# Optimization experiments

Measured on AMD Instinct MI355X. Metric: run time of the kernel, lower is better.

## Reference

```python
import jax, jax.numpy as jnp
import numpy as np

HIDDEN = 1024
NUM_HEADS = 16
HEAD_DIM = HIDDEN // NUM_HEADS
WINDOW = 512


def setup_inputs() -> dict:
    key = jax.random.key(0)
    ks = jax.random.split(key, 6)
    b, s = 2, 4096
    x = jax.random.normal(ks[0], (b, s, HIDDEN), dtype=jnp.float32)
    attention_mask = jnp.ones((b, s), dtype=jnp.int32)
    scale = 1.0 / np.sqrt(HIDDEN)
    Wq = jax.random.normal(ks[1], (HIDDEN, HIDDEN), dtype=jnp.float32) * scale
    Wk = jax.random.normal(ks[2], (HIDDEN, HIDDEN), dtype=jnp.float32) * scale
    Wv = jax.random.normal(ks[3], (HIDDEN, HIDDEN), dtype=jnp.float32) * scale
    Wo = jax.random.normal(ks[4], (HIDDEN, HIDDEN), dtype=jnp.float32) * scale
    return {"x": x, "attention_mask": attention_mask,
            "Wq": Wq, "Wk": Wk, "Wv": Wv, "Wo": Wo}


def reference(x, attention_mask, Wq, Wk, Wv, Wo):
    b, s, d = x.shape
    # nn.Linear computes x @ W.T
    q = (x @ Wq.T).reshape(b, s, NUM_HEADS, HEAD_DIM).transpose(0, 2, 1, 3)
    k = (x @ Wk.T).reshape(b, s, NUM_HEADS, HEAD_DIM).transpose(0, 2, 1, 3)
    v = (x @ Wv.T).reshape(b, s, NUM_HEADS, HEAD_DIM).transpose(0, 2, 1, 3)
    # [b,h,s,s] scores
    scores = jnp.einsum('bhqd,bhkd->bhqk', q, k) / np.sqrt(HEAD_DIM)
    # causal sliding-window mask: allow j <= i and j >= i - window + 1
    i = jnp.arange(s)[:, None]
    j = jnp.arange(s)[None, :]
    window_mask = (j <= i) & (j >= i - WINDOW + 1)  # [s,s]
    neg_inf = jnp.finfo(scores.dtype).min
    scores = jnp.where(window_mask[None, None], scores, neg_inf)
    pad = attention_mask.astype(bool)[:, None, None, :]  # [b,1,1,s]
    scores = jnp.where(pad, scores, neg_inf)
    probs = jax.nn.softmax(scores, axis=-1)
    out = jnp.einsum('bhqk,bhkd->bhqd', probs, v)
    out = out.transpose(0, 2, 1, 3).reshape(b, s, d)
    return out @ Wo.T
```

## Files before the change

kernel.cpp:

```cpp
#include <hip/hip_runtime.h>
#include <cstdint>
#include <cstddef>

#define HID 1024
#define SEQ 4096
#define NB  2
#define NH  16
#define HD  64
#define WIN 512
#define TOK (NB*SEQ)

typedef _Float16 f16x8 __attribute__((ext_vector_type(8)));
typedef _Float16 f16x4 __attribute__((ext_vector_type(4)));
typedef float    f32x4 __attribute__((ext_vector_type(4)));

__global__ __launch_bounds__(256)
void convert_kernel(const float* __restrict__ X, const float* __restrict__ w0,
                    const float* __restrict__ w1, const float* __restrict__ w2,
                    const float* __restrict__ w3,
                    _Float16* __restrict__ Xh, _Float16* __restrict__ Wh) {
  const int bi = blockIdx.x;
  const float* src; _Float16* dst; size_t off;
  if (bi < 4096) {
    src = X; dst = Xh; off = (size_t)bi * 2048;
  } else {
    const int wi = bi - 4096, z = wi >> 9;
    src = (z == 0) ? w0 : (z == 1) ? w1 : (z == 2) ? w2 : w3;
    dst = Wh + (size_t)z * HID * HID;
    off = (size_t)(wi & 511) * 2048;
  }
  const size_t i = off + (size_t)threadIdx.x * 8;
  f32x4 a = *(const f32x4*)(src + i);
  f32x4 b = *(const f32x4*)(src + i + 4);
  f16x8 o;
#pragma unroll
  for (int r = 0; r < 4; ++r) { o[r] = (_Float16)a[r]; o[r+4] = (_Float16)b[r]; }
  *(f16x8*)(dst + i) = o;
}

__device__ __forceinline__ void gload16(const void* g, void* lds) {
  __builtin_amdgcn_global_load_lds(
      (__attribute__((address_space(1))) void*)(void*)g,
      (__attribute__((address_space(3))) void*)lds, 16, 0, 0);
}

__device__ __forceinline__ void gemm_mainloop(
    const _Float16* __restrict__ A, const _Float16* __restrict__ W,
    _Float16* sA, _Float16* sB, f32x4 (&acc)[4][4], int m0, int n0) {
  const int tid  = threadIdx.x;
  const int lane = tid & 63;
  const int wave = tid >> 6;
  const int wm = wave >> 1, wn = wave & 1;
  const int l15 = lane & 15, quad = lane >> 4;

  const int o0 = tid * 16;
  const int o1 = o0 + 4096;
  const _Float16* a0 = A + (size_t)(m0 + (o0 >> 6)) * HID + ((o0 & 63) >> 1);
  const _Float16* a1 = A + (size_t)(m0 + (o1 >> 6)) * HID + ((o1 & 63) >> 1);
  const _Float16* w0 = W + (size_t)(n0 + (o0 >> 6)) * HID + ((o0 & 63) >> 1);
  const _Float16* w1 = W + (size_t)(n0 + (o1 >> 6)) * HID + ((o1 & 63) >> 1);
  _Float16* la0 = sA + (o0 >> 1);
  _Float16* la1 = sA + (o1 >> 1);
  _Float16* lb0 = sB + (o0 >> 1);
  _Float16* lb1 = sB + (o1 >> 1);

  const int aoff = (wm*64 + l15)*32 + quad*8;
  const int boff = (wn*64 + l15)*32 + quad*8;

  for (int k0 = 0; k0 < HID; k0 += 64) {
    __syncthreads();
    gload16(a0 + k0,      la0);
    gload16(a1 + k0,      la1);
    gload16(a0 + k0 + 32, la0 + 4096);
    gload16(a1 + k0 + 32, la1 + 4096);
    gload16(w0 + k0,      lb0);
    gload16(w1 + k0,      lb1);
    gload16(w0 + k0 + 32, lb0 + 4096);
    gload16(w1 + k0 + 32, lb1 + 4096);
    __syncthreads();
#pragma unroll
    for (int s = 0; s < 2; ++s) {
      const int sb = s * 4096;
      f16x8 af[4], wf[4];
#pragma unroll
      for (int t = 0; t < 4; ++t) {
        af[t] = *(const f16x8*)(sA + sb + aoff + t*512);
        wf[t] = *(const f16x8*)(sB + sb + boff + t*512);
      }
#pragma unroll
      for (int i = 0; i < 4; ++i)
#pragma unroll
        for (int j = 0; j < 4; ++j)
          acc[i][j] = __builtin_amdgcn_mfma_f32_16x16x32_f16(af[i], wf[j], acc[i][j], 0, 0, 0);
    }
  }
}

__global__ __launch_bounds__(256, 3)
void gemm_qkv_kernel(const _Float16* __restrict__ X,
                     const _Float16* __restrict__ Wh,
                     _Float16* __restrict__ Q,
                     _Float16* __restrict__ Kb,
                     _Float16* __restrict__ Vt) {
  __shared__ __align__(16) _Float16 sA[128*64];
  __shared__ __align__(16) _Float16 sB[128*64];
  const int i  = blockIdx.x;
  const int g  = i & 7;
  const int j  = i >> 3;
  const int mi = j & 7;
  const int c  = j >> 3;
  const int z  = c >> 3;
  const int n0 = (c & 7) * 128;
  const int m0 = (g*8 + mi) * 128;
  const _Float16* W = Wh + (size_t)z * HID * HID;
  f32x4 acc[4][4] = {};
  gemm_mainloop(X, W, sA, sB, acc, m0, n0);

  const int tid  = threadIdx.x;
  const int lane = tid & 63;
  const int wave = tid >> 6;
  const int wm = wave >> 1, wn = wave & 1;
  const int l15 = lane & 15, quad = lane >> 4;

  if (z < 2) {
    _Float16* C = (z == 0) ? Q : Kb;
    const float scl = (z == 0) ? 0.18033688011f : 1.0f;
#pragma unroll
    for (int tm = 0; tm < 4; ++tm)
#pragma unroll
      for (int tn = 0; tn < 4; ++tn) {
        const int row = m0 + wm*64 + tm*16 + quad*4;
        const int col = n0 + wn*64 + tn*16 + l15;
#pragma unroll
        for (int r = 0; r < 4; ++r)
          C[(size_t)(row + r)*HID + col] = (_Float16)(acc[tm][tn][r] * scl);
      }
  } else {
#pragma unroll
    for (int tm = 0; tm < 4; ++tm)
#pragma unroll
      for (int tn = 0; tn < 4; ++tn) {
        const int row = m0 + wm*64 + tm*16 + quad*4;
        const int col = n0 + wn*64 + tn*16 + l15;
        f16x4 v;
#pragma unroll
        for (int r = 0; r < 4; ++r) v[r] = (_Float16)acc[tm][tn][r];
        *(f16x4*)(Vt + (size_t)col*TOK + row) = v;
      }
  }
}

__global__ __launch_bounds__(256, 3)
void gemm_o_kernel(const _Float16* __restrict__ A,
                   const _Float16* __restrict__ Wo,
                   float* __restrict__ C) {
  __shared__ __align__(16) _Float16 sA[128*64];
  __shared__ __align__(16) _Float16 sB[128*64];
  const int i  = blockIdx.x;
  const int g  = i & 7;
  const int j  = i >> 3;
  const int mi = j & 7;
  const int n0 = (j >> 3) * 128;
  const int m0 = (g*8 + mi) * 128;
  f32x4 acc[4][4] = {};
  gemm_mainloop(A, Wo, sA, sB, acc, m0, n0);

  const int tid  = threadIdx.x;
  const int lane = tid & 63;
  const int wave = tid >> 6;
  const int wm = wave >> 1, wn = wave & 1;
  const int l15 = lane & 15, quad = lane >> 4;
#pragma unroll
  for (int tm = 0; tm < 4; ++tm)
#pragma unroll
    for (int tn = 0; tn < 4; ++tn) {
      const int row = m0 + wm*64 + tm*16 + quad*4;
      const int col = n0 + wn*64 + tn*16 + l15;
#pragma unroll
      for (int r = 0; r < 4; ++r)
        C[(size_t)(row + r)*HID + col] = acc[tm][tn][r];
    }
}

__global__ __launch_bounds__(512, 4)
void attn_kernel(const _Float16* __restrict__ Q, const _Float16* __restrict__ Kb,
                 const _Float16* __restrict__ Vt, const int* __restrict__ AM,
                 _Float16* __restrict__ O) {
  __shared__ __align__(16) _Float16 sK[128*64];
  __shared__ __align__(16) _Float16 sV[64*128];
  __shared__ __align__(16) _Float16 sP[8*32*64];
  __shared__ int sOK;

  const int bi = blockIdx.x;
  const int g  = bi & 7;
  const int jj = bi >> 3;
  const int combo = g*4 + (jj >> 4);
  const int h = combo & 15, b = combo >> 4;
  const int qb = jj & 15;

  const int tid  = threadIdx.x;
  const int lane = tid & 63, wave = tid >> 6;
  const int l15 = lane & 15, quad = lane >> 4;

  const int q0 = qb * 256;
  const int qw = q0 + wave * 32;

  const int swz = l15 & 7;
  const int cA8 = ((quad ^ swz) << 3);
  const int cB8 = (((quad + 4) ^ swz) << 3);

  f16x8 qf[2][2];
#pragma unroll
  for (int ns = 0; ns < 2; ++ns) {
    const size_t qbse = (size_t)(b*SEQ + qw + ns*16 + l15)*HID + h*HD + quad*8;
    qf[ns][0] = *(const f16x8*)(Q + qbse);
    qf[ns][1] = *(const f16x8*)(Q + qbse + 32);
  }

  int stage_lo = (q0 - (WIN - 1));
  stage_lo = (stage_lo < 0) ? 0 : (stage_lo & ~127);
  const int nst = (q0 + 256 - stage_lo) >> 7;

  if (tid == 0) sOK = 1;
  __syncthreads();
  {
    int ok = 1;
    for (int j = stage_lo + tid; j < q0 + 256; j += 512) ok &= (AM[b*SEQ + j] != 0);
    if (!ok) sOK = 0;
  }
  __syncthreads();
  const bool allok = (sOK != 0);

  const int prow = tid >> 3;
  const int pc   = tid & 7;
  const int pco  = ((pc ^ (prow & 7)) << 3);
  f16x8 pk0, pk1, pv0, pv1;
  {
    const _Float16* kp = Kb + (size_t)(b*SEQ + stage_lo + prow)*HID + h*HD + pco;
    pk0 = *(const f16x8*)kp;
    pk1 = *(const f16x8*)(kp + (size_t)64*HID);
    const _Float16* vp = Vt + (size_t)(h*HD + prow)*TOK + b*SEQ + stage_lo + pco;
    pv0 = *(const f16x8*)vp;
    pv1 = *(const f16x8*)(vp + 64);
  }

  float l_run[2] = {0.0f, 0.0f};
  f32x4 o[4][2] = {};
  _Float16* myP = sP + wave * (32*64);

  for (int st = 0; st < nst; ++st) {
    const int j0st = stage_lo + st*128;
    __syncthreads();
    *(f16x8*)(sK + prow*64 + pc*8)        = pk0;
    *(f16x8*)(sK + (64 + prow)*64 + pc*8) = pk1;
    *(f16x8*)(sV + prow*128 + pc*8)       = pv0;
    *(f16x8*)(sV + prow*128 + 64 + pc*8)  = pv1;
    __syncthreads();
    if (st + 1 < nst) {
      const int jn = j0st + 128;
      const _Float16* kp = Kb + (size_t)(b*SEQ + jn + prow)*HID + h*HD + pco;
      pk0 = *(const f16x8*)kp;
      pk1 = *(const f16x8*)(kp + (size_t)64*HID);
      const _Float16* vp = Vt + (size_t)(h*HD + prow)*TOK + b*SEQ + jn + pco;
      pv0 = *(const f16x8*)vp;
      pv1 = *(const f16x8*)(vp + 64);
    }

#pragma unroll
    for (int s = 0; s < 2; ++s) {
      const int j0 = j0st + s*64;
      if (j0 > qw + 31 || j0 + 63 < qw - (WIN - 1)) continue;
      const bool interior = (j0 + 63 <= qw) && (j0 >= qw - (WIN - 32));

      f32x4 sc[4][2] = {};
#pragma unroll
      for (int t = 0; t < 4; ++t) {
        const f16x8 kf0 = *(const f16x8*)(sK + (s*64 + t*16 + l15)*64 + cA8);
        const f16x8 kf1 = *(const f16x8*)(sK + (s*64 + t*16 + l15)*64 + cB8);
        sc[t][0] = __builtin_amdgcn_mfma_f32_16x16x32_f16(kf0, qf[0][0], sc[t][0], 0, 0, 0);
        sc[t][0] = __builtin_amdgcn_mfma_f32_16x16x32_f16(kf1, qf[0][1], sc[t][0], 0, 0, 0);
        sc[t][1] = __builtin_amdgcn_mfma_f32_16x16x32_f16(kf0, qf[1][0], sc[t][1], 0, 0, 0);
        sc[t][1] = __builtin_amdgcn_mfma_f32_16x16x32_f16(kf1, qf[1][1], sc[t][1], 0, 0, 0);
      }

      if (!allok) {
#pragma unroll
        for (int t = 0; t < 4; ++t)
#pragma unroll
          for (int r = 0; r < 4; ++r) {
            const float ad = (AM[b*SEQ + j0 + t*16 + quad*4 + r] == 0) ? -2e30f : 0.0f;
            sc[t][0][r] += ad;
            sc[t][1][r] += ad;
          }
      }

#pragma unroll
      for (int ns = 0; ns < 2; ++ns) {
        if (!interior) {
          const int i = qw + ns*16 + l15;
#pragma unroll
          for (int t = 0; t < 4; ++t)
#pragma unroll
            for (int r = 0; r < 4; ++r) {
              const int j = j0 + t*16 + quad*4 + r;
              const bool valid = (unsigned)(i - j) < WIN;
              sc[t][ns][r] = valid ? sc[t][ns][r] : -1e30f;
            }
        }
        float sum = 0.0f;
#pragma unroll
        for (int t = 0; t < 4; ++t) {
          f16x4 pvv;
#pragma unroll
          for (int r = 0; r < 4; ++r) {
            const float p = __builtin_amdgcn_exp2f(sc[t][ns][r]);
            sum += p;
            pvv[r] = (_Float16)p;
          }
          const int paddr = (ns*16 + l15)*64 + (((2*t + (quad >> 1)) ^ swz) << 3) + (quad & 1)*4;
          *(f16x4*)(myP + paddr) = pvv;
        }
        sum += __shfl_xor(sum, 16, 64);
        sum += __shfl_xor(sum, 32, 64);
        l_run[ns] += sum;
      }

      const f16x8 pf00 = *(const f16x8*)(myP + l15*64 + cA8);
      const f16x8 pf01 = *(const f16x8*)(myP + l15*64 + cB8);
      const f16x8 pf10 = *(const f16x8*)(myP + (16 + l15)*64 + cA8);
      const f16x8 pf11 = *(const f16x8*)(myP + (16 + l15)*64 + cB8);
#pragma unroll
      for (int dt = 0; dt < 4; ++dt) {
        const f16x8 vf0 = *(const f16x8*)(sV + (dt*16 + l15)*128 + s*64 + cA8);
        const f16x8 vf1 = *(const f16x8*)(sV + (dt*16 + l15)*128 + s*64 + cB8);
        o[dt][0] = __builtin_amdgcn_mfma_f32_16x16x32_f16(vf0, pf00, o[dt][0], 0, 0, 0);
        o[dt][0] = __builtin_amdgcn_mfma_f32_16x16x32_f16(vf1, pf01, o[dt][0], 0, 0, 0);
        o[dt][1] = __builtin_amdgcn_mfma_f32_16x16x32_f16(vf0, pf10, o[dt][1], 0, 0, 0);
        o[dt][1] = __builtin_amdgcn_mfma_f32_16x16x32_f16(vf1, pf11, o[dt][1], 0, 0, 0);
      }
    }
  }

  const float inv[2] = {1.0f / fmaxf(l_run[0], 1e-30f), 1.0f / fmaxf(l_run[1], 1e-30f)};
#pragma unroll
  for (int ns = 0; ns < 2; ++ns) {
    const size_t ob = (size_t)(b*SEQ + qw + ns*16 + l15)*HID + h*HD + quad*4;
#pragma unroll
    for (int dt = 0; dt < 4; ++dt) {
      f16x4 v;
#pragma unroll
      for (int r = 0; r < 4; ++r) v[r] = (_Float16)(o[dt][ns][r] * inv[ns]);
      *(f16x4*)(O + ob + dt*16) = v;
    }
  }
}

extern "C" void kernel_launch(void* const* d_in, const int* in_sizes, int n_in,
                              void* d_out, int out_size, void* d_ws, size_t ws_size,
                              hipStream_t stream) {
  const float* X  = (const float*)d_in[0];
  const int*   AM = (const int*)d_in[1];
  const float* Wq = (const float*)d_in[2];
  const float* Wk = (const float*)d_in[3];
  const float* Wv = (const float*)d_in[4];
  const float* Wo = (const float*)d_in[5];
  float* out = (float*)d_out;

  _Float16* Xh = (_Float16*)d_ws;
  _Float16* Wh = Xh + (size_t)TOK*HID;
  _Float16* Qb = Wh + (size_t)4*HID*HID;
  _Float16* Kb = Qb + (size_t)TOK*HID;
  _Float16* Vt = Kb + (size_t)TOK*HID;
  _Float16* AO = Vt + (size_t)TOK*HID;

  convert_kernel<<<dim3(4096 + 4*512), dim3(256), 0, stream>>>(X, Wq, Wk, Wv, Wo, Xh, Wh);
  gemm_qkv_kernel<<<dim3(1536), dim3(256), 0, stream>>>(Xh, Wh, Qb, Kb, Vt);
  attn_kernel<<<dim3(512), dim3(512), 0, stream>>>(Qb, Kb, Vt, AM, AO);
  gemm_o_kernel<<<dim3(512), dim3(256), 0, stream>>>(AO, Wh + (size_t)3*HID*HID, out);
}
```

Measured before the change: 217.6 us.

## Load K/V fragments directly from global per wave, drop shared staging

The attention kernel no longer stages K and V tiles through shared memory with block-wide barriers. Each wave now loads its K and V MFMA fragments straight from global memory (relying on L2 for reuse) and walks only the 64-key tiles in its own window. Blocks shrink to 256 threads covering 128 queries, with 1024 blocks, and the padding-mask check becomes a per-wave vote. This removes the barriers and LDS traffic, but each wave loads K/V redundantly, there is no prefetch across iterations, and the K rows are read with strided global accesses.

Result: slower. 274.6 us (+26.2%).

```diff
diff --git a/kernel.cpp b/kernel.cpp
--- a/kernel.cpp
+++ b/kernel.cpp
@@ -182,28 +182,24 @@
     }
 }
 
-__global__ __launch_bounds__(512, 4)
+__global__ __launch_bounds__(256, 3)
 void attn_kernel(const _Float16* __restrict__ Q, const _Float16* __restrict__ Kb,
                  const _Float16* __restrict__ Vt, const int* __restrict__ AM,
                  _Float16* __restrict__ O) {
-  __shared__ __align__(16) _Float16 sK[128*64];
-  __shared__ __align__(16) _Float16 sV[64*128];
-  __shared__ __align__(16) _Float16 sP[8*32*64];
-  __shared__ int sOK;
+  __shared__ __align__(16) _Float16 sP[4*32*64];
 
   const int bi = blockIdx.x;
   const int g  = bi & 7;
   const int jj = bi >> 3;
-  const int combo = g*4 + (jj >> 4);
+  const int combo = g*4 + (jj >> 5);
   const int h = combo & 15, b = combo >> 4;
-  const int qb = jj & 15;
+  const int qt = jj & 31;
 
   const int tid  = threadIdx.x;
   const int lane = tid & 63, wave = tid >> 6;
   const int l15 = lane & 15, quad = lane >> 4;
 
-  const int q0 = qb * 256;
-  const int qw = q0 + wave * 32;
+  const int qw = qt*128 + wave*32;
 
   const int swz = l15 & 7;
   const int cA8 = ((quad ^ swz) << 3);
@@ -217,127 +213,99 @@
     qf[ns][1] = *(const f16x8*)(Q + qbse + 32);
   }
 
-  int stage_lo = (q0 - (WIN - 1));
-  stage_lo = (stage_lo < 0) ? 0 : (stage_lo & ~127);
-  const int nst = (q0 + 256 - stage_lo) >> 7;
-
-  if (tid == 0) sOK = 1;
-  __syncthreads();
-  {
-    int ok = 1;
-    for (int j = stage_lo + tid; j < q0 + 256; j += 512) ok &= (AM[b*SEQ + j] != 0);
-    if (!ok) sOK = 0;
-  }
-  __syncthreads();
-  const bool allok = (sOK != 0);
-
-  const int prow = tid >> 3;
-  const int pc   = tid & 7;
-  const int pco  = ((pc ^ (prow & 7)) << 3);
-  f16x8 pk0, pk1, pv0, pv1;
-  {
-    const _Float16* kp = Kb + (size_t)(b*SEQ + stage_lo + prow)*HID + h*HD + pco;
-    pk0 = *(const f16x8*)kp;
-    pk1 = *(const f16x8*)(kp + (size_t)64*HID);
-    const _Float16* vp = Vt + (size_t)(h*HD + prow)*TOK + b*SEQ + stage_lo + pco;
-    pv0 = *(const f16x8*)vp;
-    pv1 = *(const f16x8*)(vp + 64);
-  }
+  int lo = qw - (WIN - 1); if (lo < 0) lo = 0;
+  const int kt_lo = lo >> 6;
+  const int kt_hi = (qw + 31) >> 6;
+
+  int okl = 1;
+  for (int j = kt_lo*64 + lane; j < (kt_hi + 1)*64; j += 64)
+    okl &= (AM[b*SEQ + j] != 0);
+  const bool allok = __all(okl);
 
   float l_run[2] = {0.0f, 0.0f};
   f32x4 o[4][2] = {};
   _Float16* myP = sP + wave * (32*64);
 
-  for (int st = 0; st < nst; ++st) {
-    const int j0st = stage_lo + st*128;
-    __syncthreads();
-    *(f16x8*)(sK + prow*64 + pc*8)        = pk0;
-    *(f16x8*)(sK + (64 + prow)*64 + pc*8) = pk1;
-    *(f16x8*)(sV + prow*128 + pc*8)       = pv0;
-    *(f16x8*)(sV + prow*128 + 64 + pc*8)  = pv1;
-    __syncthreads();
-    if (st + 1 < nst) {
-      const int jn = j0st + 128;
-      const _Float16* kp = Kb + (size_t)(b*SEQ + jn + prow)*HID + h*HD + pco;
-      pk0 = *(const f16x8*)kp;
-      pk1 = *(const f16x8*)(kp + (size_t)64*HID);
-      const _Float16* vp = Vt + (size_t)(h*HD + prow)*TOK + b*SEQ + jn + pco;
-      pv0 = *(const f16x8*)vp;
-      pv1 = *(const f16x8*)(vp + 64);
-    }
-
-#pragma unroll
-    for (int s = 0; s < 2; ++s) {
-      const int j0 = j0st + s*64;
-      if (j0 > qw + 31 || j0 + 63 < qw - (WIN - 1)) continue;
-      const bool interior = (j0 + 63 <= qw) && (j0 >= qw - (WIN - 32));
-
-      f32x4 sc[4][2] = {};
+  for (int kt = kt_lo; kt <= kt_hi; ++kt) {
+    const int j0 = kt * 64;
+    const bool interior = (j0 + 63 <= qw) && (j0 >= qw - (WIN - 32));
+
+    f16x8 kf[4][2];
+#pragma unroll
+    for (int t = 0; t < 4; ++t) {
+      const _Float16* kp = Kb + (size_t)(b*SEQ + j0 + t*16 + l15)*HID + h*HD + quad*8;
+      kf[t][0] = *(const f16x8*)kp;
+      kf[t][1] = *(const f16x8*)(kp + 32);
+    }
+    f16x8 vf[4][2];
+#pragma unroll
+    for (int dt = 0; dt < 4; ++dt) {
+      const _Float16* vp = Vt + (size_t)(h*HD + dt*16 + l15)*TOK + b*SEQ + j0 + quad*8;
+      vf[dt][0] = *(const f16x8*)vp;
+      vf[dt][1] = *(const f16x8*)(vp + 32);
+    }
+
+    f32x4 sc[4][2] = {};
+#pragma unroll
+    for (int t = 0; t < 4; ++t) {
+      sc[t][0] = __builtin_amdgcn_mfma_f32_16x16x32_f16(kf[t][0], qf[0][0], sc[t][0], 0, 0, 0);
+      sc[t][0] = __builtin_amdgcn_mfma_f32_16x16x32_f16(kf[t][1], qf[0][1], sc[t][0], 0, 0, 0);
+      sc[t][1] = __builtin_amdgcn_mfma_f32_16x16x32_f16(kf[t][0], qf[1][0], sc[t][1], 0, 0, 0);
+      sc[t][1] = __builtin_amdgcn_mfma_f32_16x16x32_f16(kf[t][1], qf[1][1], sc[t][1], 0, 0, 0);
+    }
+
+    if (!allok) {
+#pragma unroll
+      for (int t = 0; t < 4; ++t)
+#pragma unroll
+        for (int r = 0; r < 4; ++r) {
+          const float ad = (AM[b*SEQ + j0 + t*16 + quad*4 + r] == 0) ? -2e30f : 0.0f;
+          sc[t][0][r] += ad;
+          sc[t][1][r] += ad;
+        }
+    }
+
+#pragma unroll
+    for (int ns = 0; ns < 2; ++ns) {
+      if (!interior) {
+        const int i = qw + ns*16 + l15;
+#pragma unroll
+        for (int t = 0; t < 4; ++t)
+#pragma unroll
+          for (int r = 0; r < 4; ++r) {
+            const int j = j0 + t*16 + quad*4 + r;
+            const bool valid = (unsigned)(i - j) < WIN;
+            sc[t][ns][r] = valid ? sc[t][ns][r] : -1e30f;
+          }
+      }
+      float sum = 0.0f;
 #pragma unroll
       for (int t = 0; t < 4; ++t) {
-        const f16x8 kf0 = *(const f16x8*)(sK + (s*64 + t*16 + l15)*64 + cA8);
-        const f16x8 kf1 = *(const f16x8*)(sK + (s*64 + t*16 + l15)*64 + cB8);
-        sc[t][0] = __builtin_amdgcn_mfma_f32_16x16x32_f16(kf0, qf[0][0], sc[t][0], 0, 0, 0);
-        sc[t][0] = __builtin_amdgcn_mfma_f32_16x16x32_f16(kf1, qf[0][1], sc[t][0], 0, 0, 0);
-        sc[t][1] = __builtin_amdgcn_mfma_f32_16x16x32_f16(kf0, qf[1][0], sc[t][1], 0, 0, 0);
-        sc[t][1] = __builtin_amdgcn_mfma_f32_16x16x32_f16(kf1, qf[1][1], sc[t][1], 0, 0, 0);
-      }
-
-      if (!allok) {
-#pragma unroll
-        for (int t = 0; t < 4; ++t)
-#pragma unroll
-          for (int r = 0; r < 4; ++r) {
-            const float ad = (AM[b*SEQ + j0 + t*16 + quad*4 + r] == 0) ? -2e30f : 0.0f;
-            sc[t][0][r] += ad;
-            sc[t][1][r] += ad;
-          }
-      }
-
-#pragma unroll
-      for (int ns = 0; ns < 2; ++ns) {
-        if (!interior) {
-          const int i = qw + ns*16 + l15;
-#pragma unroll
-          for (int t = 0; t < 4; ++t)
-#pragma unroll
-            for (int r = 0; r < 4; ++r) {
-              const int j = j0 + t*16 + quad*4 + r;
-              const bool valid = (unsigned)(i - j) < WIN;
-              sc[t][ns][r] = valid ? sc[t][ns][r] : -1e30f;
-            }
+        f16x4 pvv;
+#pragma unroll
+        for (int r = 0; r < 4; ++r) {
+          const float p = __builtin_amdgcn_exp2f(sc[t][ns][r]);
+          sum += p;
+          pvv[r] = (_Float16)p;
         }
-        float sum = 0.0f;
-#pragma unroll
-        for (int t = 0; t < 4; ++t) {
-          f16x4 pvv;
-#pragma unroll
-          for (int r = 0; r < 4; ++r) {
-            const float p = __builtin_amdgcn_exp2f(sc[t][ns][r]);
-            sum += p;
-            pvv[r] = (_Float16)p;
-          }
-          const int paddr = (ns*16 + l15)*64 + (((2*t + (quad >> 1)) ^ swz) << 3) + (quad & 1)*4;
-          *(f16x4*)(myP + paddr) = pvv;
-        }
-        sum += __shfl_xor(sum, 16, 64);
-        sum += __shfl_xor(sum, 32, 64);
-        l_run[ns] += sum;
-      }
-
-      const f16x8 pf00 = *(const f16x8*)(myP + l15*64 + cA8);
-      const f16x8 pf01 = *(const f16x8*)(myP + l15*64 + cB8);
-      const f16x8 pf10 = *(const f16x8*)(myP + (16 + l15)*64 + cA8);
-      const f16x8 pf11 = *(const f16x8*)(myP + (16 + l15)*64 + cB8);
-#pragma unroll
-      for (int dt = 0; dt < 4; ++dt) {
-        const f16x8 vf0 = *(const f16x8*)(sV + (dt*16 + l15)*128 + s*64 + cA8);
-        const f16x8 vf1 = *(const f16x8*)(sV + (dt*16 + l15)*128 + s*64 + cB8);
-        o[dt][0] = __builtin_amdgcn_mfma_f32_16x16x32_f16(vf0, pf00, o[dt][0], 0, 0, 0);
-        o[dt][0] = __builtin_amdgcn_mfma_f32_16x16x32_f16(vf1, pf01, o[dt][0], 0, 0, 0);
-        o[dt][1] = __builtin_amdgcn_mfma_f32_16x16x32_f16(vf0, pf10, o[dt][1], 0, 0, 0);
-        o[dt][1] = __builtin_amdgcn_mfma_f32_16x16x32_f16(vf1, pf11, o[dt][1], 0, 0, 0);
-      }
+        const int paddr = (ns*16 + l15)*64 + (((2*t + (quad >> 1)) ^ swz) << 3) + (quad & 1)*4;
+        *(f16x4*)(myP + paddr) = pvv;
+      }
+      sum += __shfl_xor(sum, 16, 64);
+      sum += __shfl_xor(sum, 32, 64);
+      l_run[ns] += sum;
+    }
+
+    const f16x8 pf00 = *(const f16x8*)(myP + l15*64 + cA8);
+    const f16x8 pf01 = *(const f16x8*)(myP + l15*64 + cB8);
+    const f16x8 pf10 = *(const f16x8*)(myP + (16 + l15)*64 + cA8);
+    const f16x8 pf11 = *(const f16x8*)(myP + (16 + l15)*64 + cB8);
+#pragma unroll
+    for (int dt = 0; dt < 4; ++dt) {
+      o[dt][0] = __builtin_amdgcn_mfma_f32_16x16x32_f16(vf[dt][0], pf00, o[dt][0], 0, 0, 0);
+      o[dt][0] = __builtin_amdgcn_mfma_f32_16x16x32_f16(vf[dt][1], pf01, o[dt][0], 0, 0, 0);
+      o[dt][1] = __builtin_amdgcn_mfma_f32_16x16x32_f16(vf[dt][0], pf10, o[dt][1], 0, 0, 0);
+      o[dt][1] = __builtin_amdgcn_mfma_f32_16x16x32_f16(vf[dt][1], pf11, o[dt][1], 0, 0, 0);
     }
   }
 
@@ -375,6 +343,6 @@
 
   convert_kernel<<<dim3(4096 + 4*512), dim3(256), 0, stream>>>(X, Wq, Wk, Wv, Wo, Xh, Wh);
   gemm_qkv_kernel<<<dim3(1536), dim3(256), 0, stream>>>(Xh, Wh, Qb, Kb, Vt);
-  attn_kernel<<<dim3(512), dim3(512), 0, stream>>>(Qb, Kb, Vt, AM, AO);
+  attn_kernel<<<dim3(1024), dim3(256), 0, stream>>>(Qb, Kb, Vt, AM, AO);
   gemm_o_kernel<<<dim3(512), dim3(256), 0, stream>>>(AO, Wh + (size_t)3*HID*HID, out);
 }
```
